# Optimization experiments

Hardware: AMD Instinct MI355X
Metric: run time of the kernel (lower is better)

Reference implementation:

```python
import jax, jax.numpy as jnp
import numpy as np

N = 100000
E = 3200000
D_IN = 83
D_HID = 1024
N_CLASSES = 25


def setup_inputs() -> dict:
    key = jax.random.key(0)
    ks = jax.random.split(key, 10)
    feature = jax.random.normal(ks[0], (N, D_IN), dtype=jnp.float32)
    edge_row = jax.random.randint(ks[1], (E,), 0, N, dtype=jnp.int32)
    edge_col = jax.random.randint(ks[2], (E,), 0, N, dtype=jnp.int32)
    adj_val = jax.random.uniform(ks[3], (E,), dtype=jnp.float32)
    # Conv1d(1 -> 4, kernel 5, pad 2): weight [out=4, in=1, k=5]
    conv_w = jax.random.normal(ks[4], (4, 1, 5), dtype=jnp.float32) * 0.2
    conv_b = jnp.zeros((4,), dtype=jnp.float32)
    # GCN weights (kaiming-uniform-like scale), zero biases
    W1 = jax.random.uniform(ks[5], (D_IN, D_HID), dtype=jnp.float32,
                            minval=-1.0, maxval=1.0) * np.sqrt(6.0 / D_IN)
    b1 = jnp.zeros((D_HID,), dtype=jnp.float32)
    W2 = jax.random.uniform(ks[6], (D_HID, N_CLASSES), dtype=jnp.float32,
                            minval=-1.0, maxval=1.0) * np.sqrt(6.0 / D_HID)
    b2 = jnp.zeros((N_CLASSES,), dtype=jnp.float32)
    return {"feature": feature, "conv_w": conv_w, "conv_b": conv_b,
            "W1": W1, "b1": b1, "W2": W2, "b2": b2,
            "adj_val": adj_val, "edge_row": edge_row, "edge_col": edge_col}


def _spmm(vals, row, col, X):
    # sparse(adj) @ X : gather source rows, scale by edge value, scatter-add to dest
    return jax.ops.segment_sum(vals[:, None] * X[col], row, num_segments=N)


def reference(feature, conv_w, conv_b, W1, b1, W2, b2, adj_val, edge_row, edge_col):
    # Conv1d prelude: [N,1,83] -> [N,4,83], sum over channels, relu -> [N,83]
    x = jax.lax.conv_general_dilated(
        feature[:, None, :], conv_w, window_strides=(1,), padding=[(2, 2)],
        dimension_numbers=("NCH", "OIH", "NCH"))
    x = x + conv_b[None, :, None]
    x = jax.nn.relu(jnp.sum(x, axis=1))
    # GCN layer 1: relu(A @ (x W1) + b1)
    h = jax.nn.relu(_spmm(adj_val, edge_row, edge_col, x @ W1) + b1)
    # GCN layer 2: A @ (h W2) + b2
    logits = _spmm(adj_val, edge_row, edge_col, h @ W2) + b2
    return logits
```

## Files before the change

kernel.cpp:

```cpp
#include <hip/hip_runtime.h>

#define NN   100000
#define EE   3200000
#define DIN  83
#define DHID 1024
#define NCLS 25
#define XPAD 96
#define ZPAD 32

#define NBK     391
#define SLAB    10240
#define CHUNK   8192

typedef __attribute__((__ext_vector_type__(8))) short sh8;
typedef __attribute__((__ext_vector_type__(4))) float f4_t;

static __device__ __forceinline__ float relu_(float v) { return v > 0.f ? v : 0.f; }

static __device__ __forceinline__ unsigned short f2bf(float f) {
  unsigned int u = __float_as_uint(f);
  unsigned int r = u + 0x7FFFu + ((u >> 16) & 1u);
  return (unsigned short)(r >> 16);
}
static __device__ __forceinline__ float bflo(unsigned int q) {
  return __uint_as_float(q << 16);
}
static __device__ __forceinline__ float bfhi(unsigned int q) {
  return __uint_as_float(q & 0xFFFF0000u);
}

__global__ __launch_bounds__(256) void prelude_k(
    const float* __restrict__ feature, const float* __restrict__ conv_w,
    const float* __restrict__ conv_b, unsigned short* __restrict__ x,
    const float* __restrict__ W1, unsigned short* __restrict__ w1t,
    const float* __restrict__ W2, unsigned short* __restrict__ w2t,
    int* __restrict__ gcur) {
  int t = blockIdx.x * 256 + threadIdx.x;
  if (t < DHID * XPAD) {
    int k = t / DHID;
    int n = t - k * DHID;
    float v = (k < DIN) ? W1[k * DHID + n] : 0.f;
    w1t[n * XPAD + k] = f2bf(v);
  }
  if (t < 32 * DHID) {
    int k = t / 32;
    int n = t - k * 32;
    float v = (n < NCLS) ? W2[k * NCLS + n] : 0.f;
    w2t[n * DHID + k] = f2bf(v);
  }
  if (t < NBK * 16) gcur[t] = 0;
  if (t >= NN * 12) return;
  int n = t / 12;
  int g = t - n * 12;
  int i0 = g * 8;
  float ws0 = conv_w[0] + conv_w[5] + conv_w[10] + conv_w[15];
  float ws1 = conv_w[1] + conv_w[6] + conv_w[11] + conv_w[16];
  float ws2 = conv_w[2] + conv_w[7] + conv_w[12] + conv_w[17];
  float ws3 = conv_w[3] + conv_w[8] + conv_w[13] + conv_w[18];
  float ws4 = conv_w[4] + conv_w[9] + conv_w[14] + conv_w[19];
  float bs  = conv_b[0] + conv_b[1] + conv_b[2] + conv_b[3];
  const float* f = feature + (size_t)n * DIN;
  float fv[12];
#pragma unroll
  for (int k = 0; k < 12; ++k) {
    int idx = i0 - 2 + k;
    fv[k] = (idx >= 0 && idx < DIN) ? f[idx] : 0.f;
  }
  sh8 vout;
#pragma unroll
  for (int j = 0; j < 8; ++j) {
    int i = i0 + j;
    unsigned short o = 0;
    if (i < DIN) {
      float acc = bs + ws0 * fv[j] + ws1 * fv[j + 1] + ws2 * fv[j + 2] +
                  ws3 * fv[j + 3] + ws4 * fv[j + 4];
      o = f2bf(relu_(acc));
    }
    vout[j] = (short)o;
  }
  *(sh8*)&x[(size_t)n * XPAD + i0] = vout;
}

__global__ __launch_bounds__(256) void partition_k(
    const float* __restrict__ vals, const int* __restrict__ row,
    const int* __restrict__ col, int* __restrict__ gcur,
    int2* __restrict__ tmp) {
  __shared__ int cnt[NBK];
  __shared__ int lcur[NBK];
  const int tid = threadIdx.x;
  const int cb = blockIdx.x * CHUNK;
  const int csize = (cb + CHUNK <= EE) ? CHUNK : (EE - cb);

  for (int b = tid; b < NBK; b += 256) cnt[b] = 0;
  __syncthreads();
  for (int i = tid; i < csize; i += 256)
    atomicAdd(&cnt[row[cb + i] >> 8], 1);
  __syncthreads();
  for (int b = tid; b < NBK; b += 256)
    lcur[b] = cnt[b] ? (b * SLAB + atomicAdd(&gcur[b * 16], cnt[b])) : 0;
  __syncthreads();
  for (int i = tid; i < csize; i += 256) {
    int r = row[cb + i];
    int pos = atomicAdd(&lcur[r >> 8], 1);
    tmp[pos] = make_int2(col[cb + i] | ((r & 255) << 17),
                         __float_as_int(vals[cb + i]));
  }
}

__global__ __launch_bounds__(512) void fine_scatter2_k(
    const int* __restrict__ gcur, const int2* __restrict__ tmp,
    int2* __restrict__ csr, int* __restrict__ offs, int* __restrict__ counts) {
  __shared__ int cnt[256];
  __shared__ int sd[256];
  __shared__ int lcur[256];
  const int tid = threadIdx.x;
  const int b = blockIdx.x;
  const int r0 = b * 256;
  const int gstart = b * SLAB;
  const int nedge = gcur[b * 16];
  if (tid < 256) cnt[tid] = 0;
  __syncthreads();
  for (int i = tid; i < nedge; i += 512)
    atomicAdd(&cnt[((unsigned)tmp[gstart + i].x) >> 17], 1);
  __syncthreads();
  int v = 0;
  if (tid < 256) { v = cnt[tid]; sd[tid] = v; }
  __syncthreads();
  for (int off = 1; off < 256; off <<= 1) {
    int add = (tid >= off && tid < 256) ? sd[tid - off] : 0;
    __syncthreads();
    if (tid < 256) sd[tid] += add;
    __syncthreads();
  }
  if (tid < 256) {
    int excl = gstart + sd[tid] - v;
    int r = r0 + tid;
    if (r < NN) {
      offs[r] = excl;
      counts[r] = v;
    }
    lcur[tid] = excl;
  }
  __syncthreads();
  for (int i = tid; i < nedge; i += 512) {
    int2 p = tmp[gstart + i];
    int rl = ((unsigned)p.x) >> 17;
    int pos = atomicAdd(&lcur[rl], 1);
    csr[pos] = make_int2(p.x & 0x1FFFF, p.y);
  }
}

__global__ __launch_bounds__(256) void spmm83_g(
    const int* __restrict__ offs, const int* __restrict__ cnt,
    const int2* __restrict__ csr, const unsigned short* __restrict__ x,
    unsigned short* __restrict__ ax) {
  int wave = (int)((blockIdx.x * blockDim.x + threadIdx.x) >> 6);
  int lane = threadIdx.x & 63;
  if (wave >= NN) return;
  int s = __builtin_amdgcn_readfirstlane(offs[wave]);
  int n = __builtin_amdgcn_readfirstlane(cnt[wave]);
  const bool act = lane < 48;
  const int d2 = lane * 2;
  float a0 = 0.f, a1 = 0.f;
  int i = 0;
  for (; i + 16 <= n; i += 16) {
    int2 p[16];
#pragma unroll
    for (int u = 0; u < 16; ++u) p[u] = csr[s + i + u];
    if (act) {
      unsigned int q[16];
#pragma unroll
      for (int u = 0; u < 16; ++u)
        q[u] = *(const unsigned int*)&x[(size_t)p[u].x * XPAD + d2];
#pragma unroll
      for (int u = 0; u < 16; ++u) {
        float v = __int_as_float(p[u].y);
        a0 += v * bflo(q[u]);
        a1 += v * bfhi(q[u]);
      }
    }
  }
  for (; i + 8 <= n; i += 8) {
    int2 p[8];
#pragma unroll
    for (int u = 0; u < 8; ++u) p[u] = csr[s + i + u];
    if (act) {
      unsigned int q[8];
#pragma unroll
      for (int u = 0; u < 8; ++u)
        q[u] = *(const unsigned int*)&x[(size_t)p[u].x * XPAD + d2];
#pragma unroll
      for (int u = 0; u < 8; ++u) {
        float v = __int_as_float(p[u].y);
        a0 += v * bflo(q[u]);
        a1 += v * bfhi(q[u]);
      }
    }
  }
  for (; i < n; ++i) {
    int2 p = csr[s + i];
    if (act) {
      unsigned int q = *(const unsigned int*)&x[(size_t)p.x * XPAD + d2];
      float v = __int_as_float(p.y);
      a0 += v * bflo(q);
      a1 += v * bfhi(q);
    }
  }
  if (act) {
    unsigned int o = (unsigned int)f2bf(a0) | ((unsigned int)f2bf(a1) << 16);
    *(unsigned int*)&ax[(size_t)wave * XPAD + d2] = o;
  }
}

__global__ __launch_bounds__(256) void spmm25_g(
    const int* __restrict__ offs, const int* __restrict__ cnt,
    const int2* __restrict__ csr, const unsigned short* __restrict__ zb,
    const float* __restrict__ b2, float* __restrict__ out) {
  int gw = (int)((blockIdx.x * blockDim.x + threadIdx.x) >> 6);
  int lane = threadIdx.x & 63;
  int sub = lane >> 4;
  int d2 = (lane & 15) * 2;
  int r = gw * 4 + sub;
  if (r >= NN) return;
  int s = offs[r];
  int n = cnt[r];
  float a0 = 0.f, a1 = 0.f;
  int i = 0;
  for (; i + 8 <= n; i += 8) {
    int2 p[8];
#pragma unroll
    for (int u = 0; u < 8; ++u) p[u] = csr[s + i + u];
    unsigned int q[8];
#pragma unroll
    for (int u = 0; u < 8; ++u)
      q[u] = *(const unsigned int*)&zb[(size_t)p[u].x * ZPAD + d2];
#pragma unroll
    for (int u = 0; u < 8; ++u) {
      float v = __int_as_float(p[u].y);
      a0 += v * bflo(q[u]);
      a1 += v * bfhi(q[u]);
    }
  }
  for (; i < n; ++i) {
    int2 p = csr[s + i];
    unsigned int q = *(const unsigned int*)&zb[(size_t)p.x * ZPAD + d2];
    float v = __int_as_float(p.y);
    a0 += v * bflo(q);
    a1 += v * bfhi(q);
  }
  if (d2 < NCLS)     out[(size_t)r * NCLS + d2]     = a0 + b2[d2];
  if (d2 + 1 < NCLS) out[(size_t)r * NCLS + d2 + 1] = a1 + b2[d2 + 1];
}

__global__ __launch_bounds__(256) void fused_mlp_mfma(
    const unsigned short* __restrict__ axg, const unsigned short* __restrict__ w1t,
    const float* __restrict__ b1, const unsigned short* __restrict__ w2t,
    unsigned short* __restrict__ zb) {
  __shared__ __align__(16) unsigned short axs[128 * 104];
  __shared__ __align__(16) unsigned short hs[128 * 136];
  __shared__ float b1s[DHID];
  const int tid = threadIdx.x;
  const int n0 = blockIdx.x * 128;

  for (int idx = tid; idx < 128 * 12; idx += 256) {
    int m = idx / 12;
    int c8 = idx - m * 12;
    int node = n0 + m;
    sh8 v = {0, 0, 0, 0, 0, 0, 0, 0};
    if (node < NN) v = *(const sh8*)&axg[(size_t)node * XPAD + c8 * 8];
    *(sh8*)&axs[m * 104 + c8 * 8] = v;
  }
  for (int i = tid; i < DHID; i += 256) b1s[i] = b1[i];
  __syncthreads();

  const int lane = tid & 63;
  const int w = tid >> 6;
  const int quad = lane >> 4;
  const int tn = lane & 15;
  const int mta = w;
  const int mtb = w + 4;

  sh8 a1[8][3];
#pragma unroll
  for (int mt = 0; mt < 8; ++mt)
#pragma unroll
    for (int kc = 0; kc < 3; ++kc)
      a1[mt][kc] = *(const sh8*)&axs[(mt * 16 + tn) * 104 + kc * 32 + quad * 8];

  f4_t za0 = {0.f, 0.f, 0.f, 0.f}, za1 = {0.f, 0.f, 0.f, 0.f};
  f4_t zb0 = {0.f, 0.f, 0.f, 0.f}, zb1 = {0.f, 0.f, 0.f, 0.f};

  for (int c = 0; c < 8; ++c) {
    const int cb = c * 128;
#pragma unroll
    for (int nti = 0; nti < 2; ++nti) {
      const int nt = w * 2 + nti;
      const int ng = cb + nt * 16 + tn;
      const unsigned short* wr = &w1t[(size_t)ng * XPAD + quad * 8];
      sh8 b0 = *(const sh8*)&wr[0];
      sh8 b1f = *(const sh8*)&wr[32];
      sh8 b2f = *(const sh8*)&wr[64];
      float bias = b1s[ng];
#pragma unroll
      for (int mt = 0; mt < 8; ++mt) {
        f4_t acc = {0.f, 0.f, 0.f, 0.f};
        acc = __builtin_amdgcn_mfma_f32_16x16x32_bf16(a1[mt][0], b0, acc, 0, 0, 0);
        acc = __builtin_amdgcn_mfma_f32_16x16x32_bf16(a1[mt][1], b1f, acc, 0, 0, 0);
        acc = __builtin_amdgcn_mfma_f32_16x16x32_bf16(a1[mt][2], b2f, acc, 0, 0, 0);
#pragma unroll
        for (int r = 0; r < 4; ++r) {
          float v = relu_(acc[r] + bias);
          hs[(mt * 16 + quad * 4 + r) * 136 + nt * 16 + tn] = f2bf(v);
        }
      }
    }
    __syncthreads();
#pragma unroll
    for (int kc = 0; kc < 4; ++kc) {
      sh8 bl = *(const sh8*)&w2t[(size_t)tn * DHID + cb + kc * 32 + quad * 8];
      sh8 bh = *(const sh8*)&w2t[(size_t)(16 + tn) * DHID + cb + kc * 32 + quad * 8];
      sh8 aa = *(const sh8*)&hs[(mta * 16 + tn) * 136 + kc * 32 + quad * 8];
      za0 = __builtin_amdgcn_mfma_f32_16x16x32_bf16(aa, bl, za0, 0, 0, 0);
      za1 = __builtin_amdgcn_mfma_f32_16x16x32_bf16(aa, bh, za1, 0, 0, 0);
      sh8 ab = *(const sh8*)&hs[(mtb * 16 + tn) * 136 + kc * 32 + quad * 8];
      zb0 = __builtin_amdgcn_mfma_f32_16x16x32_bf16(ab, bl, zb0, 0, 0, 0);
      zb1 = __builtin_amdgcn_mfma_f32_16x16x32_bf16(ab, bh, zb1, 0, 0, 0);
    }
    __syncthreads();
  }

#pragma unroll
  for (int r = 0; r < 4; ++r) {
    int na = n0 + mta * 16 + quad * 4 + r;
    if (na < NN) {
      zb[(size_t)na * ZPAD + tn]      = f2bf(za0[r]);
      zb[(size_t)na * ZPAD + 16 + tn] = f2bf(za1[r]);
    }
    int nb = n0 + mtb * 16 + quad * 4 + r;
    if (nb < NN) {
      zb[(size_t)nb * ZPAD + tn]      = f2bf(zb0[r]);
      zb[(size_t)nb * ZPAD + 16 + tn] = f2bf(zb1[r]);
    }
  }
}

extern "C" void kernel_launch(void* const* d_in, const int* in_sizes, int n_in,
                              void* d_out, int out_size, void* d_ws, size_t ws_size,
                              hipStream_t stream) {
  const float* feature = (const float*)d_in[0];
  const float* conv_w  = (const float*)d_in[1];
  const float* conv_b  = (const float*)d_in[2];
  const float* W1      = (const float*)d_in[3];
  const float* b1      = (const float*)d_in[4];
  const float* W2      = (const float*)d_in[5];
  const float* b2      = (const float*)d_in[6];
  const float* adj     = (const float*)d_in[7];
  const int*   erow    = (const int*)d_in[8];
  const int*   ecol    = (const int*)d_in[9];
  float* out = (float*)d_out;

  char* B = (char*)d_ws;
  size_t o = 0;
  auto alloc = [&](size_t bytes, size_t align) -> void* {
    o = (o + align - 1) & ~(align - 1);
    void* p = B + o;
    o += bytes;
    return p;
  };
  unsigned short* x    = (unsigned short*)alloc((size_t)NN * XPAD * 2, 16);
  unsigned short* ax   = (unsigned short*)alloc((size_t)NN * XPAD * 2, 16);
  unsigned short* zb   = (unsigned short*)alloc((size_t)NN * ZPAD * 2, 16);
  int*   counts  = (int*)alloc((size_t)NN * 4, 16);
  int*   offs    = (int*)alloc((size_t)NN * 4, 16);
  int*   gcur    = (int*)alloc((size_t)NBK * 16 * 4, 64);
  unsigned short* w1t = (unsigned short*)alloc((size_t)DHID * XPAD * 2, 16);
  unsigned short* w2t = (unsigned short*)alloc((size_t)32 * DHID * 2, 16);
  int2*  tmp     = (int2*)alloc((size_t)NBK * SLAB * 8, 16);
  int2*  csr     = (int2*)alloc((size_t)NBK * SLAB * 8, 16);

  prelude_k<<<(NN * 12 + 255) / 256, 256, 0, stream>>>(
      feature, conv_w, conv_b, x, W1, w1t, W2, w2t, gcur);
  partition_k<<<(EE + CHUNK - 1) / CHUNK, 256, 0, stream>>>(adj, erow, ecol, gcur, tmp);
  fine_scatter2_k<<<NBK, 512, 0, stream>>>(gcur, tmp, csr, offs, counts);
  spmm83_g<<<(NN + 3) / 4, 256, 0, stream>>>(offs, counts, csr, x, ax);
  fused_mlp_mfma<<<(NN + 127) / 128, 256, 0, stream>>>(ax, w1t, b1, w2t, zb);
  spmm25_g<<<(NN + 15) / 16, 256, 0, stream>>>(offs, counts, csr, zb, b2, out);
}
```

Measured before the change: 442.2 us.

## Count per-row degrees with global atomics in partition and stage conv features in LDS

Per-row edge counts are now built in partition_k with a global atomicAdd per edge. This removes fine_scatter2_k's separate histogram pass over the temporary edge buffer, so that kernel reads the precomputed counts for its scan. The conv prelude now loads 16 feature rows per block cooperatively into shared memory, making the global reads coalesced instead of each thread reading overlapping strided windows. The trade-off is 3.2M random-address global atomics, which contend at L2 and may cost more than the LDS histogram pass they replace.

```diff
diff --git a/kernel.cpp b/kernel.cpp
--- a/kernel.cpp
+++ b/kernel.cpp
@@ -34,8 +34,9 @@
     const float* __restrict__ conv_b, unsigned short* __restrict__ x,
     const float* __restrict__ W1, unsigned short* __restrict__ w1t,
     const float* __restrict__ W2, unsigned short* __restrict__ w2t,
-    int* __restrict__ gcur) {
-  int t = blockIdx.x * 256 + threadIdx.x;
+    int* __restrict__ gcur, int* __restrict__ counts) {
+  const int tid = threadIdx.x;
+  int t = blockIdx.x * 256 + tid;
   if (t < DHID * XPAD) {
     int k = t / DHID;
     int n = t - k * DHID;
@@ -49,9 +50,20 @@
     w2t[n * DHID + k] = f2bf(v);
   }
   if (t < NBK * 16) gcur[t] = 0;
-  if (t >= NN * 12) return;
-  int n = t / 12;
-  int g = t - n * 12;
+  if (t < NN) counts[t] = 0;
+  const int nb0 = blockIdx.x * 16;
+  if (nb0 >= NN) return;
+  __shared__ float fs[16 * 84];
+  const size_t base = (size_t)nb0 * DIN;
+  for (int i = tid; i < 16 * DIN; i += 256) {
+    int nl = i / DIN;
+    int dd = i - nl * DIN;
+    fs[nl * 84 + dd] = feature[base + i];
+  }
+  __syncthreads();
+  if (tid >= 192) return;
+  int nl = tid / 12;
+  int g = tid - nl * 12;
   int i0 = g * 8;
   float ws0 = conv_w[0] + conv_w[5] + conv_w[10] + conv_w[15];
   float ws1 = conv_w[1] + conv_w[6] + conv_w[11] + conv_w[16];
@@ -59,7 +71,7 @@
   float ws3 = conv_w[3] + conv_w[8] + conv_w[13] + conv_w[18];
   float ws4 = conv_w[4] + conv_w[9] + conv_w[14] + conv_w[19];
   float bs  = conv_b[0] + conv_b[1] + conv_b[2] + conv_b[3];
-  const float* f = feature + (size_t)n * DIN;
+  const float* f = &fs[nl * 84];
   float fv[12];
 #pragma unroll
   for (int k = 0; k < 12; ++k) {
@@ -78,13 +90,13 @@
     }
     vout[j] = (short)o;
   }
-  *(sh8*)&x[(size_t)n * XPAD + i0] = vout;
+  *(sh8*)&x[(size_t)(nb0 + nl) * XPAD + i0] = vout;
 }
 
 __global__ __launch_bounds__(256) void partition_k(
     const float* __restrict__ vals, const int* __restrict__ row,
     const int* __restrict__ col, int* __restrict__ gcur,
-    int2* __restrict__ tmp) {
+    int2* __restrict__ tmp, int* __restrict__ counts) {
   __shared__ int cnt[NBK];
   __shared__ int lcur[NBK];
   const int tid = threadIdx.x;
@@ -93,8 +105,11 @@
 
   for (int b = tid; b < NBK; b += 256) cnt[b] = 0;
   __syncthreads();
-  for (int i = tid; i < csize; i += 256)
-    atomicAdd(&cnt[row[cb + i] >> 8], 1);
+  for (int i = tid; i < csize; i += 256) {
+    int r = row[cb + i];
+    atomicAdd(&cnt[r >> 8], 1);
+    atomicAdd(&counts[r], 1);
+  }
   __syncthreads();
   for (int b = tid; b < NBK; b += 256)
     lcur[b] = cnt[b] ? (b * SLAB + atomicAdd(&gcur[b * 16], cnt[b])) : 0;
@@ -108,9 +123,9 @@
 }
 
 __global__ __launch_bounds__(512) void fine_scatter2_k(
-    const int* __restrict__ gcur, const int2* __restrict__ tmp,
-    int2* __restrict__ csr, int* __restrict__ offs, int* __restrict__ counts) {
-  __shared__ int cnt[256];
+    const int* __restrict__ gcur, const int* __restrict__ counts,
+    const int2* __restrict__ tmp, int2* __restrict__ csr,
+    int* __restrict__ offs) {
   __shared__ int sd[256];
   __shared__ int lcur[256];
   const int tid = threadIdx.x;
@@ -118,13 +133,12 @@
   const int r0 = b * 256;
   const int gstart = b * SLAB;
   const int nedge = gcur[b * 16];
-  if (tid < 256) cnt[tid] = 0;
-  __syncthreads();
-  for (int i = tid; i < nedge; i += 512)
-    atomicAdd(&cnt[((unsigned)tmp[gstart + i].x) >> 17], 1);
-  __syncthreads();
   int v = 0;
-  if (tid < 256) { v = cnt[tid]; sd[tid] = v; }
+  if (tid < 256) {
+    int r = r0 + tid;
+    v = (r < NN) ? counts[r] : 0;
+    sd[tid] = v;
+  }
   __syncthreads();
   for (int off = 1; off < 256; off <<= 1) {
     int add = (tid >= off && tid < 256) ? sd[tid - off] : 0;
@@ -135,10 +149,7 @@
   if (tid < 256) {
     int excl = gstart + sd[tid] - v;
     int r = r0 + tid;
-    if (r < NN) {
-      offs[r] = excl;
-      counts[r] = v;
-    }
+    if (r < NN) offs[r] = excl;
     lcur[tid] = excl;
   }
   __syncthreads();
@@ -378,10 +389,12 @@
   int2*  tmp     = (int2*)alloc((size_t)NBK * SLAB * 8, 16);
   int2*  csr     = (int2*)alloc((size_t)NBK * SLAB * 8, 16);
 
-  prelude_k<<<(NN * 12 + 255) / 256, 256, 0, stream>>>(
-      feature, conv_w, conv_b, x, W1, w1t, W2, w2t, gcur);
-  partition_k<<<(EE + CHUNK - 1) / CHUNK, 256, 0, stream>>>(adj, erow, ecol, gcur, tmp);
-  fine_scatter2_k<<<NBK, 512, 0, stream>>>(gcur, tmp, csr, offs, counts);
+  const int nblk_prelude = (NN + 15) / 16;
+  prelude_k<<<nblk_prelude, 256, 0, stream>>>(
+      feature, conv_w, conv_b, x, W1, w1t, W2, w2t, gcur, counts);
+  partition_k<<<(EE + CHUNK - 1) / CHUNK, 256, 0, stream>>>(
+      adj, erow, ecol, gcur, tmp, counts);
+  fine_scatter2_k<<<NBK, 512, 0, stream>>>(gcur, counts, tmp, csr, offs);
   spmm83_g<<<(NN + 3) / 4, 256, 0, stream>>>(offs, counts, csr, x, ax);
   fused_mlp_mfma<<<(NN + 127) / 128, 256, 0, stream>>>(ax, w1t, b1, w2t, zb);
   spmm25_g<<<(NN + 15) / 16, 256, 0, stream>>>(offs, counts, csr, zb, b2, out);
```

Measured after the change: 545.0 us. 23.2% more time.
